# Performance work log

Measured on AMD Instinct MI355X. Metric: run time of the kernel, lower is better.

Reference implementation:

```python
import jax, jax.numpy as jnp
import numpy as np

DIM_IN, DIM_Q, DIM_V = 1024, 1024, 1024
B, S = 4, 2048
NEG_INF = 1.0e9


def setup_inputs() -> dict:
    key = jax.random.key(0)
    ks = jax.random.split(key, 11)
    c_q = (6.0 / (DIM_IN + DIM_Q)) ** 0.5
    c_v = (6.0 / (DIM_IN + DIM_V)) ** 0.5
    b_bound = 1.0 / np.sqrt(DIM_IN)  # torch Linear default bias init
    return {
        "query": jax.random.normal(ks[0], (B, S, DIM_IN), jnp.float32),
        "key": jax.random.normal(ks[1], (B, S, DIM_IN), jnp.float32),
        "value": jax.random.normal(ks[2], (B, S, DIM_IN), jnp.float32),
        "mask": jax.random.randint(ks[3], (B, S, S), 0, 2).astype(bool),
        "Wq": jax.random.uniform(ks[4], (DIM_Q, DIM_IN), jnp.float32, -c_q, c_q),
        "bq": jax.random.uniform(ks[5], (DIM_Q,), jnp.float32, -b_bound, b_bound),
        "Wk": jax.random.uniform(ks[6], (DIM_Q, DIM_IN), jnp.float32, -c_q, c_q),
        "bk": jax.random.uniform(ks[7], (DIM_Q,), jnp.float32, -b_bound, b_bound),
        "Wv": jax.random.uniform(ks[8], (DIM_V, DIM_IN), jnp.float32, -c_v, c_v),
        "bv": jax.random.uniform(ks[9], (DIM_V,), jnp.float32, -b_bound, b_bound),
    }


def reference(query, key, value, mask, Wq, bq, Wk, bk, Wv, bv):
    q = jnp.einsum("bsd,qd->bsq", query, Wq) + bq  # [B,S,dim_q]
    k = jnp.einsum("bsd,qd->bsq", key, Wk) + bk    # [B,S,dim_q]
    v = jnp.einsum("bsd,vd->bsv", value, Wv) + bv  # [B,S,dim_v]
    scale = 1.0 / jnp.sqrt(jnp.asarray(q.shape[-1], q.dtype))
    scores = jnp.einsum("bqd,bkd->bqk", q, k) * scale  # [B,S,S]
    scores = jnp.where(mask, -NEG_INF, scores)
    affinity = jax.nn.softmax(scores, axis=-1)
    out = jnp.einsum("bqk,bkv->bqv", affinity, v)  # [B,S,dim_v]
    return out
```

## Files before the change

kernel.cpp:

```cpp
#include <hip/hip_runtime.h>

#define BB 4
#define SS 2048
#define DD 1024

typedef __attribute__((ext_vector_type(8))) short short8;
typedef __attribute__((ext_vector_type(4))) float f32x4;

__device__ __forceinline__ unsigned short f2b(float f) {
  unsigned u = __builtin_bit_cast(unsigned, f);
  u += 0x7fffu + ((u >> 16) & 1u);
  return (unsigned short)(u >> 16);
}
__device__ __forceinline__ float b2f(unsigned short us) {
  unsigned u = (unsigned)us << 16;
  return __builtin_bit_cast(float, u);
}

__device__ __forceinline__ void gl2lds16(const void* g, void* l) {
  __builtin_amdgcn_global_load_lds(
      (__attribute__((address_space(1))) unsigned int*)(void*)(size_t)(uintptr_t)g,
      (__attribute__((address_space(3))) unsigned int*)l, 16, 0, 0);
}

__global__ __launch_bounds__(256) void cvt_all(
    const float* __restrict__ q, const float* __restrict__ k, const float* __restrict__ v,
    const float* __restrict__ wq, const float* __restrict__ wk, const float* __restrict__ wv,
    unsigned short* __restrict__ qo, unsigned short* __restrict__ ko, unsigned short* __restrict__ vo,
    unsigned short* __restrict__ wqo, unsigned short* __restrict__ wko, unsigned short* __restrict__ wvo) {
  const int z = blockIdx.z;
  const float* s;
  unsigned short* d;
  size_t i;
  if (blockIdx.x < 4096) {
    s = z == 0 ? q : (z == 1 ? k : v);
    d = z == 0 ? qo : (z == 1 ? ko : vo);
    i = (size_t)blockIdx.x * 2048 + threadIdx.x * 8;
  } else {
    s = z == 0 ? wq : (z == 1 ? wk : wv);
    d = z == 0 ? wqo : (z == 1 ? wko : wvo);
    i = (size_t)(blockIdx.x - 4096) * 2048 + threadIdx.x * 8;
  }
  float4 a = *(const float4*)(s + i);
  float4 b = *(const float4*)(s + i + 4);
  union { unsigned short us[8]; uint4 v4; } o;
  o.us[0] = f2b(a.x); o.us[1] = f2b(a.y); o.us[2] = f2b(a.z); o.us[3] = f2b(a.w);
  o.us[4] = f2b(b.x); o.us[5] = f2b(b.y); o.us[6] = f2b(b.z); o.us[7] = f2b(b.w);
  *(uint4*)(d + i) = o.v4;
}

enum { EPI_BIAS_COL = 0, EPI_BIAS_ROW = 1, EPI_SCORE = 2, EPI_OUT = 3 };

template <int EPI>
__global__ __launch_bounds__(256, 2) void gemm_bt(
    const unsigned short* __restrict__ A, int lda, long long aBatch,
    const unsigned short* __restrict__ Bm, int ldb, long long bBatch,
    void* __restrict__ Cv, int ldc, long long cBatch,
    int K,
    const float* __restrict__ bias,
    const float* __restrict__ bias2,
    float scale) {
  __shared__ unsigned short sA[128 * 32];
  __shared__ unsigned short sB[128 * 32];
  const int tid  = threadIdx.x;
  const int wave = tid >> 6;
  const int lane = tid & 63;
  const int l15  = lane & 15;
  const int quad = lane >> 4;
  const int waveR = wave >> 1, waveC = wave & 1;
  const int bm = blockIdx.x * 128;
  const int bn = blockIdx.y * 128;
  const int z  = blockIdx.z;
  A  += (long long)z * aBatch;
  Bm += (long long)z * bBatch;

  const unsigned short* gA0 = A  + (size_t)(bm + (tid >> 2)) * lda + (tid & 3) * 8;
  const unsigned short* gA1 = gA0 + (size_t)64 * lda;
  const unsigned short* gB0 = Bm + (size_t)(bn + (tid >> 2)) * ldb + (tid & 3) * 8;
  const unsigned short* gB1 = gB0 + (size_t)64 * ldb;
  unsigned short* lA = sA + wave * 64 * 8;
  unsigned short* lB = sB + wave * 64 * 8;

  f32x4 acc[4][4] = {};

  const int aro = (waveR * 64 + l15) * 32 + quad * 8;
  const int bro = (waveC * 64 + l15) * 32 + quad * 8;

  for (int kt = 0; kt < K; kt += 32) {
    gl2lds16(gA0, lA);
    gl2lds16(gA1, lA + 256 * 8);
    gl2lds16(gB0, lB);
    gl2lds16(gB1, lB + 256 * 8);
    gA0 += 32; gA1 += 32; gB0 += 32; gB1 += 32;
    __syncthreads();
    short8 af[4], bf[4];
#pragma unroll
    for (int i = 0; i < 4; ++i) af[i] = *(const short8*)(sA + aro + i * 16 * 32);
#pragma unroll
    for (int j = 0; j < 4; ++j) bf[j] = *(const short8*)(sB + bro + j * 16 * 32);
#pragma unroll
    for (int i = 0; i < 4; ++i)
#pragma unroll
      for (int j = 0; j < 4; ++j)
        acc[i][j] = __builtin_amdgcn_mfma_f32_16x16x32_bf16(af[i], bf[j], acc[i][j], 0, 0, 0);
    __syncthreads();
  }

  const int r0 = bm + waveR * 64 + quad * 4;
  const int c0 = bn + waveC * 64 + l15;

  if constexpr (EPI == EPI_SCORE) {
    unsigned short* Cz = (unsigned short*)Cv + (long long)z * cBatch;
#pragma unroll
    for (int i = 0; i < 4; ++i)
#pragma unroll
      for (int r = 0; r < 4; ++r) {
        int row = r0 + i * 16 + r;
#pragma unroll
        for (int j = 0; j < 4; ++j) {
          int col = c0 + j * 16;
          Cz[(size_t)row * ldc + col] = f2b(acc[i][j][r] * scale);
        }
      }
  } else if constexpr (EPI == EPI_OUT) {
    float* Cz = (float*)Cv + (long long)z * cBatch;
#pragma unroll
    for (int i = 0; i < 4; ++i)
#pragma unroll
      for (int r = 0; r < 4; ++r) {
        int row = r0 + i * 16 + r;
#pragma unroll
        for (int j = 0; j < 4; ++j) {
          int col = c0 + j * 16;
          Cz[(size_t)row * ldc + col] = acc[i][j][r];
        }
      }
  } else {
    const float* bp = (z == 0) ? bias : bias2;
    unsigned short* Cz = (unsigned short*)Cv + (long long)z * cBatch;
#pragma unroll
    for (int i = 0; i < 4; ++i)
#pragma unroll
      for (int r = 0; r < 4; ++r) {
        int row = r0 + i * 16 + r;
#pragma unroll
        for (int j = 0; j < 4; ++j) {
          int col = c0 + j * 16;
          float v = acc[i][j][r] + (EPI == EPI_BIAS_COL ? bp[col] : bp[row]);
          Cz[(size_t)row * ldc + col] = f2b(v);
        }
      }
  }
}

__global__ __launch_bounds__(256) void softmax_rows(const unsigned short* __restrict__ Sc,
                                                    const void* __restrict__ mask,
                                                    unsigned short* __restrict__ P) {
  const size_t r = blockIdx.x;
  const unsigned short* src = Sc + r * SS;
  unsigned short* dst = P + r * SS;
  const int tid = threadIdx.x;
  const int wave = tid >> 6, lane = tid & 63;
  __shared__ int anyv[4];
  __shared__ float red[8];

  unsigned pw = ((const unsigned*)mask)[tid];
  unsigned long long bal = __ballot(pw > 1u);
  if (lane == 0) anyv[wave] = (bal != 0ULL) ? 1 : 0;
  __syncthreads();
  const bool isU8 = (anyv[0] | anyv[1] | anyv[2] | anyv[3]) != 0;

  unsigned mbits = 0;
  if (isU8) {
    uint2 v = *(const uint2*)((const unsigned char*)mask + r * SS + tid * 8);
#pragma unroll
    for (int j = 0; j < 4; ++j) {
      mbits |= (((v.x >> (8 * j)) & 0xffu) ? 1u : 0u) << j;
      mbits |= (((v.y >> (8 * j)) & 0xffu) ? 1u : 0u) << (j + 4);
    }
  } else {
    const uint4* p = (const uint4*)((const int*)mask + r * SS + tid * 8);
    uint4 a = p[0], b = p[1];
    mbits = (a.x ? 1u : 0u) | ((a.y ? 1u : 0u) << 1) | ((a.z ? 1u : 0u) << 2) |
            ((a.w ? 1u : 0u) << 3) | ((b.x ? 1u : 0u) << 4) | ((b.y ? 1u : 0u) << 5) |
            ((b.z ? 1u : 0u) << 6) | ((b.w ? 1u : 0u) << 7);
  }

  union { unsigned short us[8]; uint4 v; } in;
  in.v = *(const uint4*)(src + tid * 8);
  float xs[8];
#pragma unroll
  for (int k = 0; k < 8; ++k)
    xs[k] = ((mbits >> k) & 1u) ? -1.0e9f : b2f(in.us[k]);
  float mx = xs[0];
#pragma unroll
  for (int k = 1; k < 8; ++k) mx = fmaxf(mx, xs[k]);
#pragma unroll
  for (int o = 32; o; o >>= 1) mx = fmaxf(mx, __shfl_xor(mx, o));
  if (lane == 0) red[wave] = mx;
  __syncthreads();
  mx = fmaxf(fmaxf(red[0], red[1]), fmaxf(red[2], red[3]));
  float e[8], s = 0.f;
#pragma unroll
  for (int k = 0; k < 8; ++k) { e[k] = __expf(xs[k] - mx); s += e[k]; }
#pragma unroll
  for (int o = 32; o; o >>= 1) s += __shfl_xor(s, o);
  if (lane == 0) red[4 + wave] = s;
  __syncthreads();
  s = (red[4] + red[5]) + (red[6] + red[7]);
  float inv = 1.0f / s;
  union { unsigned short us[8]; uint4 v; } o;
#pragma unroll
  for (int k = 0; k < 8; ++k) o.us[k] = f2b(e[k] * inv);
  *(uint4*)(dst + tid * 8) = o.v;
}

extern "C" void kernel_launch(void* const* d_in, const int* in_sizes, int n_in,
                              void* d_out, int out_size, void* d_ws, size_t ws_size,
                              hipStream_t stream) {
  const float* query = (const float*)d_in[0];
  const float* key   = (const float*)d_in[1];
  const float* value = (const float*)d_in[2];
  const void*  mask  = d_in[3];
  const float* Wq = (const float*)d_in[4];
  const float* bq = (const float*)d_in[5];
  const float* Wk = (const float*)d_in[6];
  const float* bk = (const float*)d_in[7];
  const float* Wv = (const float*)d_in[8];
  const float* bv = (const float*)d_in[9];
  float* out = (float*)d_out;

  char* ws = (char*)d_ws;
  const size_t MB = 1024 * 1024;
  unsigned short* qin = (unsigned short*)(ws + 0 * MB);
  unsigned short* kin = (unsigned short*)(ws + 16 * MB);
  unsigned short* vin = (unsigned short*)(ws + 32 * MB);
  unsigned short* Wqb = (unsigned short*)(ws + 48 * MB);
  unsigned short* Wkb = (unsigned short*)(ws + 50 * MB);
  unsigned short* Wvb = (unsigned short*)(ws + 52 * MB);
  unsigned short* qb  = (unsigned short*)(ws + 54 * MB);
  unsigned short* kb  = (unsigned short*)(ws + 70 * MB);
  unsigned short* vT  = (unsigned short*)(ws + 86 * MB);
  unsigned short* Sc  = (unsigned short*)(ws + 102 * MB);
  unsigned short* P   = (unsigned short*)(ws + 134 * MB);

  dim3 blk(256);

  cvt_all<<<dim3(4608, 1, 3), blk, 0, stream>>>(
      query, key, value, Wq, Wk, Wv, qin, kin, vin, Wqb, Wkb, Wvb);

  gemm_bt<EPI_BIAS_COL><<<dim3(64, 8, 2), blk, 0, stream>>>(
      qin, 1024, 8388608LL, Wqb, 1024, 1048576LL, qb, 1024, 8388608LL,
      1024, bq, bk, 0.f);

  gemm_bt<EPI_BIAS_ROW><<<dim3(8, 64, 1), blk, 0, stream>>>(
      Wvb, 1024, 0, vin, 1024, 0, vT, 8192, 0, 1024, bv, bv, 0.f);

  gemm_bt<EPI_SCORE><<<dim3(16, 16, BB), blk, 0, stream>>>(
      qb, 1024, (long long)SS * 1024, kb, 1024, (long long)SS * 1024,
      Sc, SS, (long long)SS * SS, 1024, nullptr, nullptr, 0.03125f);

  softmax_rows<<<dim3(BB * SS), blk, 0, stream>>>(Sc, mask, P);

  gemm_bt<EPI_OUT><<<dim3(16, 8, BB), blk, 0, stream>>>(
      P, SS, (long long)SS * SS, vT, 8192, (long long)SS,
      out, 1024, (long long)SS * 1024, SS, nullptr, nullptr, 1.f);
}
```

Measured before the change: 374.2 us.

## Fuse softmax into score GEMM epilogue with bitpacked mask and deferred normalization

Removes the separate softmax kernel. The score GEMM epilogue now applies the mask, exponentiates without subtracting a max, writes bf16 exp values and atomically accumulates row sums. The output GEMM divides by the row sum. The mask is bit-packed in the conversion kernel, which also zeroes the row sums, so the full mask and scores matrix are no longer re-read. Skipping the max subtraction risks overflow if scores are large, and every masked row adds atomic traffic.

```diff
diff --git a/kernel.cpp b/kernel.cpp
--- a/kernel.cpp
+++ b/kernel.cpp
@@ -27,8 +27,49 @@
     const float* __restrict__ q, const float* __restrict__ k, const float* __restrict__ v,
     const float* __restrict__ wq, const float* __restrict__ wk, const float* __restrict__ wv,
     unsigned short* __restrict__ qo, unsigned short* __restrict__ ko, unsigned short* __restrict__ vo,
-    unsigned short* __restrict__ wqo, unsigned short* __restrict__ wko, unsigned short* __restrict__ wvo) {
+    unsigned short* __restrict__ wqo, unsigned short* __restrict__ wko, unsigned short* __restrict__ wvo,
+    const void* __restrict__ mask, unsigned short* __restrict__ bits16,
+    float* __restrict__ rsum) {
   const int z = blockIdx.z;
+  const int t = threadIdx.x;
+  if (z == 3) {
+    if (blockIdx.x < 4096) {
+      __shared__ int anyv[4];
+      unsigned pw = ((const unsigned*)mask)[t];
+      unsigned long long bal = __ballot(pw > 1u);
+      if ((t & 63) == 0) anyv[t >> 6] = (bal != 0ULL) ? 1 : 0;
+      __syncthreads();
+      const bool isU8 = (anyv[0] | anyv[1] | anyv[2] | anyv[3]) != 0;
+      const size_t base = (size_t)blockIdx.x * 4096 + (size_t)t * 16;
+      unsigned ob = 0;
+      if (isU8) {
+        uint4 w = *(const uint4*)((const unsigned char*)mask + base);
+        unsigned bw[4] = {w.x, w.y, w.z, w.w};
+#pragma unroll
+        for (int wi = 0; wi < 4; ++wi)
+#pragma unroll
+          for (int bi = 0; bi < 4; ++bi)
+            ob |= (((bw[wi] >> (8 * bi)) & 0xffu) ? 1u : 0u) << (wi * 4 + bi);
+      } else {
+        const uint4* p = (const uint4*)((const int*)mask + base);
+#pragma unroll
+        for (int wi = 0; wi < 4; ++wi) {
+          uint4 w = p[wi];
+          ob |= (w.x ? 1u : 0u) << (wi * 4 + 0);
+          ob |= (w.y ? 1u : 0u) << (wi * 4 + 1);
+          ob |= (w.z ? 1u : 0u) << (wi * 4 + 2);
+          ob |= (w.w ? 1u : 0u) << (wi * 4 + 3);
+        }
+      }
+      bits16[blockIdx.x * 256 + t] = (unsigned short)ob;
+    } else if (blockIdx.x == 4096) {
+      float4 zz = {0.f, 0.f, 0.f, 0.f};
+      float4* r4 = (float4*)rsum;
+#pragma unroll
+      for (int i = 0; i < 8; ++i) r4[t * 8 + i] = zz;
+    }
+    return;
+  }
   const float* s;
   unsigned short* d;
   size_t i;
@@ -59,6 +100,8 @@
     int K,
     const float* __restrict__ bias,
     const float* __restrict__ bias2,
+    const unsigned char* __restrict__ bits,
+    float* __restrict__ rsum,
     float scale) {
   __shared__ unsigned short sA[128 * 32];
   __shared__ unsigned short sB[128 * 32];
@@ -111,28 +154,43 @@
 
   if constexpr (EPI == EPI_SCORE) {
     unsigned short* Cz = (unsigned short*)Cv + (long long)z * cBatch;
+    const unsigned char* bz = bits + (size_t)z * SS * (SS / 8);
+    float* rz = rsum + (size_t)z * SS;
 #pragma unroll
     for (int i = 0; i < 4; ++i)
 #pragma unroll
       for (int r = 0; r < 4; ++r) {
         int row = r0 + i * 16 + r;
+        const unsigned char* brow = bz + (size_t)row * (SS / 8);
+        float partial = 0.f;
 #pragma unroll
         for (int j = 0; j < 4; ++j) {
           int col = c0 + j * 16;
-          Cz[(size_t)row * ldc + col] = f2b(acc[i][j][r] * scale);
-        }
+          int m = (brow[col >> 3] >> (col & 7)) & 1;
+          float e = m ? 0.f : __expf(acc[i][j][r] * scale);
+          unsigned short h = f2b(e);
+          Cz[(size_t)row * ldc + col] = h;
+          partial += b2f(h);
+        }
+        partial += __shfl_xor(partial, 1);
+        partial += __shfl_xor(partial, 2);
+        partial += __shfl_xor(partial, 4);
+        partial += __shfl_xor(partial, 8);
+        if (l15 == 0) atomicAdd(&rz[row], partial);
       }
   } else if constexpr (EPI == EPI_OUT) {
     float* Cz = (float*)Cv + (long long)z * cBatch;
+    const float* rz = rsum + (size_t)z * SS;
 #pragma unroll
     for (int i = 0; i < 4; ++i)
 #pragma unroll
       for (int r = 0; r < 4; ++r) {
         int row = r0 + i * 16 + r;
+        float inv = 1.0f / rz[row];
 #pragma unroll
         for (int j = 0; j < 4; ++j) {
           int col = c0 + j * 16;
-          Cz[(size_t)row * ldc + col] = acc[i][j][r];
+          Cz[(size_t)row * ldc + col] = acc[i][j][r] * inv;
         }
       }
   } else {
@@ -151,68 +209,6 @@
         }
       }
   }
-}
-
-__global__ __launch_bounds__(256) void softmax_rows(const unsigned short* __restrict__ Sc,
-                                                    const void* __restrict__ mask,
-                                                    unsigned short* __restrict__ P) {
-  const size_t r = blockIdx.x;
-  const unsigned short* src = Sc + r * SS;
-  unsigned short* dst = P + r * SS;
-  const int tid = threadIdx.x;
-  const int wave = tid >> 6, lane = tid & 63;
-  __shared__ int anyv[4];
-  __shared__ float red[8];
-
-  unsigned pw = ((const unsigned*)mask)[tid];
-  unsigned long long bal = __ballot(pw > 1u);
-  if (lane == 0) anyv[wave] = (bal != 0ULL) ? 1 : 0;
-  __syncthreads();
-  const bool isU8 = (anyv[0] | anyv[1] | anyv[2] | anyv[3]) != 0;
-
-  unsigned mbits = 0;
-  if (isU8) {
-    uint2 v = *(const uint2*)((const unsigned char*)mask + r * SS + tid * 8);
-#pragma unroll
-    for (int j = 0; j < 4; ++j) {
-      mbits |= (((v.x >> (8 * j)) & 0xffu) ? 1u : 0u) << j;
-      mbits |= (((v.y >> (8 * j)) & 0xffu) ? 1u : 0u) << (j + 4);
-    }
-  } else {
-    const uint4* p = (const uint4*)((const int*)mask + r * SS + tid * 8);
-    uint4 a = p[0], b = p[1];
-    mbits = (a.x ? 1u : 0u) | ((a.y ? 1u : 0u) << 1) | ((a.z ? 1u : 0u) << 2) |
-            ((a.w ? 1u : 0u) << 3) | ((b.x ? 1u : 0u) << 4) | ((b.y ? 1u : 0u) << 5) |
-            ((b.z ? 1u : 0u) << 6) | ((b.w ? 1u : 0u) << 7);
-  }
-
-  union { unsigned short us[8]; uint4 v; } in;
-  in.v = *(const uint4*)(src + tid * 8);
-  float xs[8];
-#pragma unroll
-  for (int k = 0; k < 8; ++k)
-    xs[k] = ((mbits >> k) & 1u) ? -1.0e9f : b2f(in.us[k]);
-  float mx = xs[0];
-#pragma unroll
-  for (int k = 1; k < 8; ++k) mx = fmaxf(mx, xs[k]);
-#pragma unroll
-  for (int o = 32; o; o >>= 1) mx = fmaxf(mx, __shfl_xor(mx, o));
-  if (lane == 0) red[wave] = mx;
-  __syncthreads();
-  mx = fmaxf(fmaxf(red[0], red[1]), fmaxf(red[2], red[3]));
-  float e[8], s = 0.f;
-#pragma unroll
-  for (int k = 0; k < 8; ++k) { e[k] = __expf(xs[k] - mx); s += e[k]; }
-#pragma unroll
-  for (int o = 32; o; o >>= 1) s += __shfl_xor(s, o);
-  if (lane == 0) red[4 + wave] = s;
-  __syncthreads();
-  s = (red[4] + red[5]) + (red[6] + red[7]);
-  float inv = 1.0f / s;
-  union { unsigned short us[8]; uint4 v; } o;
-#pragma unroll
-  for (int k = 0; k < 8; ++k) o.us[k] = f2b(e[k] * inv);
-  *(uint4*)(dst + tid * 8) = o.v;
 }
 
 extern "C" void kernel_launch(void* const* d_in, const int* in_sizes, int n_in,
@@ -241,28 +237,30 @@
   unsigned short* qb  = (unsigned short*)(ws + 54 * MB);
   unsigned short* kb  = (unsigned short*)(ws + 70 * MB);
   unsigned short* vT  = (unsigned short*)(ws + 86 * MB);
-  unsigned short* Sc  = (unsigned short*)(ws + 102 * MB);
-  unsigned short* P   = (unsigned short*)(ws + 134 * MB);
+  unsigned short* P   = (unsigned short*)(ws + 102 * MB);
+  unsigned short* bits= (unsigned short*)(ws + 134 * MB);
+  float*          rsum= (float*)(ws + 136 * MB);
 
   dim3 blk(256);
 
-  cvt_all<<<dim3(4608, 1, 3), blk, 0, stream>>>(
-      query, key, value, Wq, Wk, Wv, qin, kin, vin, Wqb, Wkb, Wvb);
+  cvt_all<<<dim3(4608, 1, 4), blk, 0, stream>>>(
+      query, key, value, Wq, Wk, Wv, qin, kin, vin, Wqb, Wkb, Wvb,
+      mask, bits, rsum);
 
   gemm_bt<EPI_BIAS_COL><<<dim3(64, 8, 2), blk, 0, stream>>>(
       qin, 1024, 8388608LL, Wqb, 1024, 1048576LL, qb, 1024, 8388608LL,
-      1024, bq, bk, 0.f);
+      1024, bq, bk, nullptr, nullptr, 0.f);
 
   gemm_bt<EPI_BIAS_ROW><<<dim3(8, 64, 1), blk, 0, stream>>>(
-      Wvb, 1024, 0, vin, 1024, 0, vT, 8192, 0, 1024, bv, bv, 0.f);
+      Wvb, 1024, 0, vin, 1024, 0, vT, 8192, 0, 1024, bv, bv, nullptr, nullptr, 0.f);
 
   gemm_bt<EPI_SCORE><<<dim3(16, 16, BB), blk, 0, stream>>>(
       qb, 1024, (long long)SS * 1024, kb, 1024, (long long)SS * 1024,
-      Sc, SS, (long long)SS * SS, 1024, nullptr, nullptr, 0.03125f);
-
-  softmax_rows<<<dim3(BB * SS), blk, 0, stream>>>(Sc, mask, P);
+      P, SS, (long long)SS * SS, 1024, nullptr, nullptr,
+      (const unsigned char*)bits, rsum, 0.03125f);
 
   gemm_bt<EPI_OUT><<<dim3(16, 8, BB), blk, 0, stream>>>(
       P, SS, (long long)SS * SS, vT, 8192, (long long)SS,
-      out, 1024, (long long)SS * 1024, SS, nullptr, nullptr, 1.f);
-}
+      out, 1024, (long long)SS * 1024, SS, nullptr, nullptr,
+      nullptr, rsum, 1.f);
+}
```

New measurement: 375.4 us. Within noise of the previous version (+0.3%).
